# Kernel optimization log

Hardware: AMD Instinct MI355X
Metric: run time of the kernel (lower is better)

The kernel has to match this reference:

```python
import jax, jax.numpy as jnp
import numpy as np

EPS = 1e-6
SLOPE = 0.01  # torch LeakyReLU / VNLeakyReLU default negative_slope
B = 1024      # number of graphs (segments)
N, S, V, H = 120000, 256, 64, 64


def _vn(W, x):
    # VNLinear: channel-mixing linear on (N, C, 3) vector features, W: (O, C)
    return jnp.einsum('oc,ncd->nod', W, x)


def _gv_linear(Wv1, Wv2, Ws, Wg, bg, sca, vec):
    # GVLinear: vec -> hidden vec, concat |vec| with sca, gate out_vec by sigmoid(out_sca)
    vi = _vn(Wv1, vec)                                   # (N, Hid, 3)
    vnorm = jnp.linalg.norm(vi, axis=-1)                 # (N, Hid)
    out_sca = jnp.concatenate([vnorm, sca], axis=-1) @ Ws.T   # (N, out_sca)
    out_vec = _vn(Wv2, vi)                               # (N, out_vec, 3)
    gate = jax.nn.sigmoid(out_sca @ Wg.T + bg)[..., None]
    return out_sca, gate * out_vec


def _vn_lrelu(Wd, x):
    # VNLeakyReLU: direction-gated leaky relu on vector channels
    d = _vn(Wd, x)
    dot = jnp.sum(x * d, axis=-1, keepdims=True)
    dsq = jnp.sum(d * d, axis=-1, keepdims=True)
    mask = (dot >= 0).astype(x.dtype)
    proj = x - (dot / (dsq + EPS)) * d
    return SLOPE * x + (1.0 - SLOPE) * (mask * x + (1.0 - mask) * proj)


def _lrelu(x):
    return jnp.where(x >= 0, x, SLOPE * x)


def setup_inputs() -> dict:
    key = jax.random.key(0)
    ks = jax.random.split(key, 40)
    g = lambda i, shape, s=1.0: jax.random.normal(ks[i], shape, dtype=jnp.float32) * s
    w = 0.06  # ~1/sqrt(fan_in) for fan_in 256-320
    inp = {
        'h_sca': g(0, (N, S)),
        'h_vec': g(1, (N, V, 3)),
        'pos_context': g(2, (N, 3), 3.0),
        'time_embed': g(3, (100, S), 0.05),
        # att_net: GVPerceptronVN(256,64 -> 256,64)
        'att1_Wv1': g(4, (H, V), 0.12), 'att1_Wv2': g(5, (H, H), 0.12),
        'att1_Ws': g(6, (S, S + H), w), 'att1_Wg': g(7, (H, S), w), 'att1_bg': g(8, (H,), 0.01),
        'att1_Wd': g(9, (H, H), 0.12),
        # att_net: GVLinear(256,64 -> 1,1), dim_hid = max(64,1) = 64
        'att2_Wv1': g(10, (H, H), 0.12), 'att2_Wv2': g(11, (1, H), 0.12),
        'att2_Ws': g(12, (1, S + H), w), 'att2_Wg': g(13, (1, 1), 0.5), 'att2_bg': g(14, (1,), 0.01),
        # net: GVPerceptronVN(256,64 -> 256,64)
        'net1_Wv1': g(15, (H, V), 0.12), 'net1_Wv2': g(16, (H, H), 0.12),
        'net1_Ws': g(17, (S, S + H), w), 'net1_Wg': g(18, (H, S), w), 'net1_bg': g(19, (H,), 0.01),
        'net1_Wd': g(20, (H, H), 0.12),
        # net: GVLinear(256,64 -> 256,64)
        'net2_Wv1': g(21, (H, H), 0.12), 'net2_Wv2': g(22, (S - (S - V), H), 0.12).reshape(V, H),
        'net2_Ws': g(23, (S, S + H), w), 'net2_Wg': g(24, (V, S), w), 'net2_bg': g(25, (V,), 0.01),
        't': 17,
        'batch_id': jnp.sort(jax.random.randint(ks[30], (N,), 0, B)),
    }
    return inp


def reference(h_sca, h_vec, pos_context, time_embed,
              att1_Wv1, att1_Wv2, att1_Ws, att1_Wg, att1_bg, att1_Wd,
              att2_Wv1, att2_Wv2, att2_Ws, att2_Wg, att2_bg,
              net1_Wv1, net1_Wv2, net1_Ws, net1_Wg, net1_bg, net1_Wd,
              net2_Wv1, net2_Wv2, net2_Ws, net2_Wg, net2_bg,
              t, batch_id):
    sca = h_sca + time_embed[t]          # same timestep embedding broadcast to all N nodes
    vec = h_vec

    # attention branch: GVPerceptronVN -> GVLinear(...,1,1), keep scalar output
    s, v = _gv_linear(att1_Wv1, att1_Wv2, att1_Ws, att1_Wg, att1_bg, sca, vec)
    s, v = _lrelu(s), _vn_lrelu(att1_Wd, v)
    att, _ = _gv_linear(att2_Wv1, att2_Wv2, att2_Ws, att2_Wg, att2_bg, s, v)  # (N,1)

    # feature branch: GVPerceptronVN -> GVLinear(...,in_sca,in_vec)
    s2, v2 = _gv_linear(net1_Wv1, net1_Wv2, net1_Ws, net1_Wg, net1_bg, sca, vec)
    s2, v2 = _lrelu(s2), _vn_lrelu(net1_Wd, v2)
    fs, fv = _gv_linear(net2_Wv1, net2_Wv2, net2_Ws, net2_Wg, net2_bg, s2, v2)

    # scatter_softmax over batch_id segments
    m = jax.ops.segment_max(att, batch_id, num_segments=B)
    e = jnp.exp(att - m[batch_id])
    z = jax.ops.segment_sum(e, batch_id, num_segments=B)
    w = e / z[batch_id]                  # (N,1)

    pos_focal = jax.ops.segment_sum(w * pos_context, batch_id, num_segments=B)   # (B,3)
    feat_focal = jax.ops.segment_sum(w * fs, batch_id, num_segments=B)           # (B,256)
    vec_focal = jax.ops.segment_sum(w[:, :, None] * fv, batch_id, num_segments=B)  # (B,64,3)
    return feat_focal, vec_focal, pos_focal
```

## Files before the change

kernel.cpp:

```cpp
#include <hip/hip_runtime.h>
#include <hip/hip_bf16.h>
#include <math.h>

#define NN 120000
#define NT 32
#define TPB 512
#define NBLK (NN / NT)
#define BSEG 1024

typedef __attribute__((ext_vector_type(8))) short short8;
typedef __attribute__((ext_vector_type(16))) float floatx16;

#define OFF_A1_WV1 0
#define OFF_A1_WV2 4096
#define OFF_A1_WS  8192
#define OFF_A1_WG  90112
#define OFF_A1_WD  106496
#define OFF_A2_WV1 110592
#define OFF_N1_WV1 114688
#define OFF_N1_WV2 118784
#define OFF_N1_WS  122880
#define OFF_N1_WG  204800
#define OFF_N1_WD  221184
#define OFF_N2_WV1 225280
#define OFF_N2_WV2 229376
#define OFF_N2_WS  233472
#define OFF_N2_WG  315392
#define W_TOTAL    331776

__device__ __forceinline__ unsigned short f2bf(float x) {
  __hip_bfloat16 b = __float2bfloat16(x);
  return __builtin_bit_cast(unsigned short, b);
}
__device__ __forceinline__ unsigned int f2bf2(float lo, float hi) {
  return (unsigned int)f2bf(lo) | ((unsigned int)f2bf(hi) << 16);
}
__device__ __forceinline__ float bf2f(unsigned short h) {
  return __uint_as_float(((unsigned int)h) << 16);
}
__device__ __forceinline__ float bflo(unsigned int u) { return __uint_as_float(u << 16); }
__device__ __forceinline__ float bfhi(unsigned int u) { return __uint_as_float(u & 0xffff0000u); }

struct P {
  const float *h_sca, *h_vec, *pos, *te;
  const float *a1_bg, *n1_bg, *n2_bg, *a2_Ws;
  const int *t, *bid;
  const unsigned short* wb;
  float *att, *w, *out;
};


struct CvtP { const float* src[15]; unsigned short* dst; };

__global__ __launch_bounds__(256) void cvt_kernel(CvtP c) {
  const int sizes[15] = {4096, 4096, 81920, 16384, 4096, 4096,
                         4096, 4096, 81920, 16384, 4096,
                         4096, 4096, 81920, 16384};
  int idx = blockIdx.x * 256 + threadIdx.x;
  if (idx >= W_TOTAL) return;
  int seg = 0, off = 0;
  while (idx - off >= sizes[seg]) { off += sizes[seg]; ++seg; }
  c.dst[idx] = f2bf(c.src[seg][idx - off]);
}


__device__ __forceinline__ void stage(const P& p, unsigned short* sS, unsigned short* sV,
                                      const float* te_row, int node0, int tid) {
  int i = tid >> 4, j = tid & 15;
  {
    int c0 = j * 16;
    const float4* src = (const float4*)&p.h_sca[(node0 + i) * 256 + c0];
    const float4* te4 = (const float4*)&te_row[c0];
    float4 a0 = src[0], b0 = te4[0];
    float4 a1 = src[1], b1 = te4[1];
    float4 a2 = src[2], b2 = te4[2];
    float4 a3 = src[3], b3 = te4[3];
    uint4 o0 = make_uint4(f2bf2(a0.x + b0.x, a0.y + b0.y), f2bf2(a0.z + b0.z, a0.w + b0.w),
                          f2bf2(a1.x + b1.x, a1.y + b1.y), f2bf2(a1.z + b1.z, a1.w + b1.w));
    uint4 o1 = make_uint4(f2bf2(a2.x + b2.x, a2.y + b2.y), f2bf2(a2.z + b2.z, a2.w + b2.w),
                          f2bf2(a3.x + b3.x, a3.y + b3.y), f2bf2(a3.z + b3.z, a3.w + b3.w));
    *(uint4*)&sS[i * 264 + c0] = o0;
    *(uint4*)&sS[i * 264 + c0 + 8] = o1;
  }
  {
    int c0 = j * 4;
    const float4* src = (const float4*)&p.h_vec[(node0 + i) * 192 + c0 * 3];
    float4 v0 = src[0], v1 = src[1], v2 = src[2];
    int b = (i * 3) * 72 + c0;
    *(uint2*)&sV[b]       = make_uint2(f2bf2(v0.x, v0.w), f2bf2(v1.z, v2.y));
    *(uint2*)&sV[b + 72]  = make_uint2(f2bf2(v0.y, v1.x), f2bf2(v1.w, v2.z));
    *(uint2*)&sV[b + 144] = make_uint2(f2bf2(v0.z, v1.y), f2bf2(v2.x, v2.w));
  }
}

__device__ __forceinline__ void big_gemm(const unsigned short* __restrict__ Wb,
                                         const unsigned short* sVN,
                                         const unsigned short* sX,
                                         unsigned short* sDst,
                                         int wid, int lane) {
  const int m = lane & 31, h = lane >> 5;
  const int n0 = wid * 32;
  const unsigned short* wrow = Wb + (n0 + m) * 320 + h * 8;
  short8 B[20];
#pragma unroll
  for (int k = 0; k < 8; ++k) B[k] = *(const short8*)&wrow[k * 16];
  floatx16 acc0 = {}, acc1 = {};
#pragma unroll
  for (int k = 0; k < 20; k += 2) {
    if (k + 8 < 20) B[k + 8] = *(const short8*)&wrow[(k + 8) * 16];
    if (k + 9 < 20) B[k + 9] = *(const short8*)&wrow[(k + 9) * 16];
    short8 a0, a1;
    if (k < 4)     a0 = *(const short8*)&sVN[m * 72 + k * 16 + h * 8];
    else           a0 = *(const short8*)&sX[m * 264 + (k - 4) * 16 + h * 8];
    if (k + 1 < 4) a1 = *(const short8*)&sVN[m * 72 + (k + 1) * 16 + h * 8];
    else           a1 = *(const short8*)&sX[m * 264 + (k - 3) * 16 + h * 8];
    acc0 = __builtin_amdgcn_mfma_f32_32x32x16_bf16(a0, B[k], acc0, 0, 0, 0);
    acc1 = __builtin_amdgcn_mfma_f32_32x32x16_bf16(a1, B[k + 1], acc1, 0, 0, 0);
  }
  __syncthreads();
#pragma unroll
  for (int r = 0; r < 16; ++r) {
    int row = (r & 3) + 8 * (r >> 2) + 4 * h;
    sDst[row * 264 + n0 + m] = f2bf(acc0[r] + acc1[r]);
  }
}

__device__ __forceinline__ void gate_gemm(const unsigned short* __restrict__ Wg,
                                          const float* __restrict__ bg,
                                          const unsigned short* sX,
                                          unsigned short* sG, int wid, int lane) {
  const int m = lane & 31, h = lane >> 5;
  const int n0 = wid * 32;
  const unsigned short* wrow = Wg + (n0 + m) * 256 + h * 8;
  short8 B[16];
#pragma unroll
  for (int k = 0; k < 8; ++k) B[k] = *(const short8*)&wrow[k * 16];
  float bb = bg[n0 + m];
  floatx16 acc0 = {}, acc1 = {};
#pragma unroll
  for (int k = 0; k < 16; k += 2) {
    if (k + 8 < 16) B[k + 8] = *(const short8*)&wrow[(k + 8) * 16];
    if (k + 9 < 16) B[k + 9] = *(const short8*)&wrow[(k + 9) * 16];
    short8 a0 = *(const short8*)&sX[m * 264 + k * 16 + h * 8];
    short8 a1 = *(const short8*)&sX[m * 264 + k * 16 + 16 + h * 8];
    acc0 = __builtin_amdgcn_mfma_f32_32x32x16_bf16(a0, B[k], acc0, 0, 0, 0);
    acc1 = __builtin_amdgcn_mfma_f32_32x32x16_bf16(a1, B[k + 1], acc1, 0, 0, 0);
  }
#pragma unroll
  for (int r = 0; r < 16; ++r) {
    int i = (r & 3) + 8 * (r >> 2) + 4 * h;
    float v = acc0[r] + acc1[r] + bb;
    sG[i * 64 + n0 + m] = f2bf(__builtin_amdgcn_rcpf(1.f + __expf(-v)));
  }
}

__device__ __forceinline__ void vecmm(const unsigned short* __restrict__ Wb,
                                      const unsigned short* sSrc,
                                      unsigned short* sDst,
                                      int wid, int lane) {
  if (wid >= 6) return;
  const int m = lane & 31, h = lane >> 5;
  const int nd0 = (wid >> 1) * 32, o0 = (wid & 1) * 32;
  const unsigned short* wrow = Wb + (o0 + m) * 64 + h * 8;
  short8 b0 = *(const short8*)&wrow[0];
  short8 b1 = *(const short8*)&wrow[16];
  short8 b2 = *(const short8*)&wrow[32];
  short8 b3 = *(const short8*)&wrow[48];
  floatx16 acc = {};
#pragma unroll
  for (int k0 = 0; k0 < 64; k0 += 16) {
    short8 a = *(const short8*)&sSrc[(nd0 + m) * 72 + k0 + h * 8];
    short8 b = (k0 == 0) ? b0 : (k0 == 16) ? b1 : (k0 == 32) ? b2 : b3;
    acc = __builtin_amdgcn_mfma_f32_32x32x16_bf16(a, b, acc, 0, 0, 0);
  }
#pragma unroll
  for (int r = 0; r < 16; ++r) {
    int nd = nd0 + (r & 3) + 8 * (r >> 2) + 4 * h;
    sDst[nd * 72 + o0 + m] = f2bf(acc[r]);
  }
}

__device__ __forceinline__ void vnorm(const unsigned short* sV, unsigned short* sVN, int tid) {
  if (tid >= 256) return;
  int i = tid >> 3, c0 = (tid & 7) * 8;
  int b = (i * 3) * 72 + c0;
  short8 vx = *(const short8*)&sV[b];
  short8 vy = *(const short8*)&sV[b + 72];
  short8 vz = *(const short8*)&sV[b + 144];
  unsigned int o[4];
#pragma unroll
  for (int q = 0; q < 4; ++q) {
    float x0 = bf2f((unsigned short)vx[2 * q]),     y0 = bf2f((unsigned short)vy[2 * q]),     z0 = bf2f((unsigned short)vz[2 * q]);
    float x1 = bf2f((unsigned short)vx[2 * q + 1]), y1 = bf2f((unsigned short)vy[2 * q + 1]), z1 = bf2f((unsigned short)vz[2 * q + 1]);
    o[q] = f2bf2(sqrtf(x0 * x0 + y0 * y0 + z0 * z0), sqrtf(x1 * x1 + y1 * y1 + z1 * z1));
  }
  *(uint4*)&sVN[i * 72 + c0] = make_uint4(o[0], o[1], o[2], o[3]);
}

__device__ __forceinline__ void gatemul(unsigned short* sVx, const unsigned short* sG, int tid) {
  if (tid >= 256) return;
  int i = tid >> 3, c0 = (tid & 7) * 8;
  short8 g = *(const short8*)&sG[i * 64 + c0];
  float gf[8];
#pragma unroll
  for (int j = 0; j < 8; ++j) gf[j] = bf2f((unsigned short)g[j]);
  int b = (i * 3) * 72 + c0;
#pragma unroll
  for (int d = 0; d < 3; ++d) {
    short8 v = *(const short8*)&sVx[b + d * 72];
    unsigned int o[4];
#pragma unroll
    for (int q = 0; q < 4; ++q)
      o[q] = f2bf2(bf2f((unsigned short)v[2 * q]) * gf[2 * q],
                   bf2f((unsigned short)v[2 * q + 1]) * gf[2 * q + 1]);
    *(uint4*)&sVx[b + d * 72] = make_uint4(o[0], o[1], o[2], o[3]);
  }
}

__device__ __forceinline__ void vn_lrelu(unsigned short* sVx, const unsigned short* sVd, int tid) {
  if (tid >= 256) return;
  int i = tid >> 3, c0 = (tid & 7) * 8;
  int b = (i * 3) * 72 + c0;
  short8 x0 = *(const short8*)&sVx[b];
  short8 x1 = *(const short8*)&sVx[b + 72];
  short8 x2 = *(const short8*)&sVx[b + 144];
  short8 d0 = *(const short8*)&sVd[b];
  short8 d1 = *(const short8*)&sVd[b + 72];
  short8 d2 = *(const short8*)&sVd[b + 144];
  float rx[8], ry[8], rz[8];
#pragma unroll
  for (int j = 0; j < 8; ++j) {
    float a0 = bf2f((unsigned short)x0[j]), a1 = bf2f((unsigned short)x1[j]), a2 = bf2f((unsigned short)x2[j]);
    float e0 = bf2f((unsigned short)d0[j]), e1 = bf2f((unsigned short)d1[j]), e2 = bf2f((unsigned short)d2[j]);
    float dot = a0 * e0 + a1 * e1 + a2 * e2;
    float dsq = e0 * e0 + e1 * e1 + e2 * e2;
    float f = dot >= 0.f ? 0.f : 0.99f * dot * __builtin_amdgcn_rcpf(dsq + 1e-6f);
    rx[j] = a0 - f * e0; ry[j] = a1 - f * e1; rz[j] = a2 - f * e2;
  }
  unsigned int ox[4], oy[4], oz[4];
#pragma unroll
  for (int q = 0; q < 4; ++q) {
    ox[q] = f2bf2(rx[2 * q], rx[2 * q + 1]);
    oy[q] = f2bf2(ry[2 * q], ry[2 * q + 1]);
    oz[q] = f2bf2(rz[2 * q], rz[2 * q + 1]);
  }
  *(uint4*)&sVx[b]       = make_uint4(ox[0], ox[1], ox[2], ox[3]);
  *(uint4*)&sVx[b + 72]  = make_uint4(oy[0], oy[1], oy[2], oy[3]);
  *(uint4*)&sVx[b + 144] = make_uint4(oz[0], oz[1], oz[2], oz[3]);
}

__device__ __forceinline__ void lrelu_vec(unsigned short* sS, int u, int nthr) {
  for (int cc = u; cc < NT * 32; cc += nthr) {
    int i = cc >> 5, off = (cc & 31) * 8;
    short8 v = *(short8*)&sS[i * 264 + off];
    unsigned int o[4];
#pragma unroll
    for (int q = 0; q < 4; ++q) {
      float a = bf2f((unsigned short)v[2 * q]);
      float b = bf2f((unsigned short)v[2 * q + 1]);
      a = a >= 0.f ? a : 0.01f * a;
      b = b >= 0.f ? b : 0.01f * b;
      o[q] = f2bf2(a, b);
    }
    *(uint4*)&sS[i * 264 + off] = make_uint4(o[0], o[1], o[2], o[3]);
  }
}

__device__ __forceinline__ float* out_addr(float* out, int b, int f) {
  if (f < 256) return out + b * 256 + f;
  if (f < 448) return out + 1024 * 256 + b * 192 + (f - 256);
  return out + 1024 * 256 + 1024 * 192 + b * 3 + (f - 448);
}


__global__ __launch_bounds__(TPB, 6) void att_kernel(P p) {
  __shared__ unsigned short sS[NT * 264];
  __shared__ unsigned short sVA[96 * 72], sVB[96 * 72];
  __shared__ unsigned short sGN[2304];
  unsigned short* sVN = sGN;
  unsigned short* sG = sGN;
  int tid = threadIdx.x, wid = tid >> 6, lane = tid & 63;
  int node0 = blockIdx.x * NT;
  const unsigned short* wb = p.wb;

  stage(p, sS, sVA, p.te + p.t[0] * 256, node0, tid); __syncthreads();
  vecmm(wb + OFF_A1_WV1, sVA, sVB, wid, lane); __syncthreads();
  vnorm(sVB, sVN, tid); __syncthreads();
  big_gemm(wb + OFF_A1_WS, sVN, sS, sS, wid, lane); __syncthreads();
  if (wid < 2) gate_gemm(wb + OFF_A1_WG, p.a1_bg, sS, sG, wid, lane);
  else vecmm(wb + OFF_A1_WV2, sVB, sVA, wid - 2, lane);
  __syncthreads();
  gatemul(sVA, sG, tid); __syncthreads();
  vecmm(wb + OFF_A1_WD, sVA, sVB, wid, lane); __syncthreads();
  vn_lrelu(sVA, sVB, tid); __syncthreads();
  vecmm(wb + OFF_A2_WV1, sVA, sVB, wid, lane); __syncthreads();

  int i = tid >> 4, j = tid & 15;
  float part = 0.f;
  {
    int c0 = j * 4;
    uint2 wx = *(const uint2*)&sVB[(i * 3 + 0) * 72 + c0];
    uint2 wy = *(const uint2*)&sVB[(i * 3 + 1) * 72 + c0];
    uint2 wz = *(const uint2*)&sVB[(i * 3 + 2) * 72 + c0];
    float4 ws = *(const float4*)&p.a2_Ws[c0];
    float n0 = sqrtf(bflo(wx.x) * bflo(wx.x) + bflo(wy.x) * bflo(wy.x) + bflo(wz.x) * bflo(wz.x));
    float n1 = sqrtf(bfhi(wx.x) * bfhi(wx.x) + bfhi(wy.x) * bfhi(wy.x) + bfhi(wz.x) * bfhi(wz.x));
    float n2 = sqrtf(bflo(wx.y) * bflo(wx.y) + bflo(wy.y) * bflo(wy.y) + bflo(wz.y) * bflo(wz.y));
    float n3 = sqrtf(bfhi(wx.y) * bfhi(wx.y) + bfhi(wy.y) * bfhi(wy.y) + bfhi(wz.y) * bfhi(wz.y));
    part = fmaf(ws.x, n0, part);
    part = fmaf(ws.y, n1, part);
    part = fmaf(ws.z, n2, part);
    part = fmaf(ws.w, n3, part);
  }
  {
    int k0 = j * 16;
    short8 s0 = *(const short8*)&sS[i * 264 + k0];
    short8 s1 = *(const short8*)&sS[i * 264 + k0 + 8];
    const float4* wp = (const float4*)&p.a2_Ws[64 + k0];
#pragma unroll
    for (int q = 0; q < 4; ++q) {
      float4 w4 = wp[q];
      float vv[4];
#pragma unroll
      for (int e = 0; e < 4; ++e) {
        short raw = (q < 2) ? ((q == 0) ? s0[e] : s0[4 + e]) : ((q == 2) ? s1[e] : s1[4 + e]);
        float x = bf2f((unsigned short)raw);
        vv[e] = x >= 0.f ? x : 0.01f * x;
      }
      part = fmaf(w4.x, vv[0], part);
      part = fmaf(w4.y, vv[1], part);
      part = fmaf(w4.z, vv[2], part);
      part = fmaf(w4.w, vv[3], part);
    }
  }
  part += __shfl_down(part, 8, 16);
  part += __shfl_down(part, 4, 16);
  part += __shfl_down(part, 2, 16);
  part += __shfl_down(part, 1, 16);
  if (j == 0) p.att[node0 + i] = part;
}


__global__ __launch_bounds__(256) void softmax_kernel(const float* __restrict__ att,
                                                      const int* __restrict__ bid,
                                                      float* __restrict__ w) {
  __shared__ float red[256];
  __shared__ float s_m, s_z;
  int b = blockIdx.x, tid = threadIdx.x;
  int lo = 0, hi = NN;
  while (lo < hi) { int mid = (lo + hi) >> 1; if (bid[mid] < b) lo = mid + 1; else hi = mid; }
  int start = lo;
  hi = NN;
  while (lo < hi) { int mid = (lo + hi) >> 1; if (bid[mid] < b + 1) lo = mid + 1; else hi = mid; }
  int end = lo;

  float m = -1e30f;
  for (int i = start + tid; i < end; i += 256) m = fmaxf(m, att[i]);
  red[tid] = m; __syncthreads();
  for (int s = 128; s > 0; s >>= 1) { if (tid < s) red[tid] = fmaxf(red[tid], red[tid + s]); __syncthreads(); }
  if (tid == 0) s_m = red[0];
  __syncthreads();
  m = s_m;
  float z = 0.f;
  for (int i = start + tid; i < end; i += 256) z += __expf(att[i] - m);
  red[tid] = z; __syncthreads();
  for (int s = 128; s > 0; s >>= 1) { if (tid < s) red[tid] += red[tid + s]; __syncthreads(); }
  if (tid == 0) s_z = red[0];
  __syncthreads();
  float inv = 1.f / s_z;
  for (int i = start + tid; i < end; i += 256) w[i] = __expf(att[i] - m) * inv;
}


__global__ __launch_bounds__(TPB, 6) void net_kernel(P p) {
  __shared__ unsigned short sS[NT * 264];
  __shared__ unsigned short sVA[96 * 72], sVB[96 * 72];
  __shared__ unsigned short sGN[2304];
  __shared__ float s_w[NT];
  __shared__ float s_pos[NT * 3];
  __shared__ int s_bid[NT];
  unsigned short* sVN = sGN;
  unsigned short* sG = sGN;
  int tid = threadIdx.x, wid = tid >> 6, lane = tid & 63;
  int node0 = blockIdx.x * NT;
  const unsigned short* wb = p.wb;

  stage(p, sS, sVA, p.te + p.t[0] * 256, node0, tid); __syncthreads();
  vecmm(wb + OFF_N1_WV1, sVA, sVB, wid, lane);
  if (wid >= 6) {
    int u = tid - 384;
    if (u < NT) { s_w[u] = p.w[node0 + u]; s_bid[u] = p.bid[node0 + u]; }
    for (int v = u; v < NT * 3; v += 128) s_pos[v] = p.pos[node0 * 3 + v];
  }
  __syncthreads();
  vnorm(sVB, sVN, tid); __syncthreads();
  big_gemm(wb + OFF_N1_WS, sVN, sS, sS, wid, lane); __syncthreads();
  if (wid < 2) gate_gemm(wb + OFF_N1_WG, p.n1_bg, sS, sG, wid, lane);
  else vecmm(wb + OFF_N1_WV2, sVB, sVA, wid - 2, lane);
  __syncthreads();
  if (tid < 256) gatemul(sVA, sG, tid);
  else lrelu_vec(sS, tid - 256, 256);
  __syncthreads();
  vecmm(wb + OFF_N1_WD, sVA, sVB, wid, lane); __syncthreads();
  vn_lrelu(sVA, sVB, tid); __syncthreads();
  vecmm(wb + OFF_N2_WV1, sVA, sVB, wid, lane); __syncthreads();
  vnorm(sVB, sVN, tid); __syncthreads();
  big_gemm(wb + OFF_N2_WS, sVN, sS, sS, wid, lane); __syncthreads();
  if (wid < 2) gate_gemm(wb + OFF_N2_WG, p.n2_bg, sS, sG, wid, lane);
  else vecmm(wb + OFF_N2_WV2, sVB, sVA, wid - 2, lane);
  __syncthreads();

  if (tid < 451) {
    int f = tid;
    float acc = 0.f;
    int cur = s_bid[0];
    int c = 0, d = 0;
    if (f >= 256 && f < 448) { int r = f - 256; c = r / 3; d = r - c * 3; }
    for (int i2 = 0; i2 < NT; ++i2) {
      int sg = s_bid[i2];
      if (sg != cur) { atomicAdd(out_addr(p.out, cur, f), acc); acc = 0.f; cur = sg; }
      float val;
      if (f < 256) val = bf2f(sS[i2 * 264 + f]);
      else if (f < 448)
        val = bf2f(sVA[(i2 * 3 + d) * 72 + c]) * bf2f(sG[i2 * 64 + c]);
      else val = s_pos[i2 * 3 + (f - 448)];
      acc = fmaf(s_w[i2], val, acc);
    }
    atomicAdd(out_addr(p.out, cur, f), acc);
  }
}


extern "C" void kernel_launch(void* const* d_in, const int* in_sizes, int n_in,
                              void* d_out, int out_size, void* d_ws, size_t ws_size,
                              hipStream_t stream) {
  float* ws = (float*)d_ws;
  unsigned short* wb = (unsigned short*)(ws + 2 * NN);

  CvtP c;
  c.src[0]  = (const float*)d_in[4];
  c.src[1]  = (const float*)d_in[5];
  c.src[2]  = (const float*)d_in[6];
  c.src[3]  = (const float*)d_in[7];
  c.src[4]  = (const float*)d_in[9];
  c.src[5]  = (const float*)d_in[10];
  c.src[6]  = (const float*)d_in[15];
  c.src[7]  = (const float*)d_in[16];
  c.src[8]  = (const float*)d_in[17];
  c.src[9]  = (const float*)d_in[18];
  c.src[10] = (const float*)d_in[20];
  c.src[11] = (const float*)d_in[21];
  c.src[12] = (const float*)d_in[22];
  c.src[13] = (const float*)d_in[23];
  c.src[14] = (const float*)d_in[24];
  c.dst = wb;

  P p;
  p.h_sca = (const float*)d_in[0];
  p.h_vec = (const float*)d_in[1];
  p.pos   = (const float*)d_in[2];
  p.te    = (const float*)d_in[3];
  p.a1_bg = (const float*)d_in[8];
  p.a2_Ws = (const float*)d_in[12];
  p.n1_bg = (const float*)d_in[19];
  p.n2_bg = (const float*)d_in[25];
  p.t   = (const int*)d_in[26];
  p.bid = (const int*)d_in[27];
  p.wb  = wb;
  p.att = ws;
  p.w   = ws + NN;
  p.out = (float*)d_out;

  hipMemsetAsync(d_out, 0, (size_t)out_size * sizeof(float), stream);
  cvt_kernel<<<(W_TOTAL + 255) / 256, 256, 0, stream>>>(c);
  att_kernel<<<NBLK, TPB, 0, stream>>>(p);
  softmax_kernel<<<BSEG, 256, 0, stream>>>(p.att, p.bid, p.w);
  net_kernel<<<NBLK, TPB, 0, stream>>>(p);
}
```

Measured before the change: 670.3 us.

## Double node tile to 64 with 1024-thread blocks and dynamic LDS

Raises the per-block node tile from 32 to 64 and threads per block from 512 to 1024. The GEMM helpers take extra row-block offsets so each weight fragment loaded from global memory serves twice as many nodes, and LDS becomes a single dynamic buffer with explicit offsets. The segment-sum epilogue splits each feature across two threads, one per half of the tile. The cost is more LDS per block and fewer resident blocks per CU, and the tile is hard-coded around the stage/att paths, some of which are not shown and may not all have been updated for 64 nodes.

```diff
diff --git a/kernel.cpp b/kernel.cpp
--- a/kernel.cpp
+++ b/kernel.cpp
@@ -3,10 +3,17 @@
 #include <math.h>
 
 #define NN 120000
-#define NT 32
-#define TPB 512
+#define NT 64
+#define TPB 1024
 #define NBLK (NN / NT)
 #define BSEG 1024
+
+#define L_SS   0
+#define L_SVA  16896
+#define L_SVB  30720
+#define L_SGN  44544
+#define L_END  49152
+#define LDS_BYTES (98304 + 64*4 + 192*4 + 64*4)
 
 typedef __attribute__((ext_vector_type(8))) short short8;
 typedef __attribute__((ext_vector_type(16))) float floatx16;
@@ -99,7 +106,8 @@
                                          unsigned short* sDst,
                                          int wid, int lane) {
   const int m = lane & 31, h = lane >> 5;
-  const int n0 = wid * 32;
+  const int n0 = (wid & 7) * 32, mb = (wid >> 3) * 32;
+  const int ar = mb + m;
   const unsigned short* wrow = Wb + (n0 + m) * 320 + h * 8;
   short8 B[20];
 #pragma unroll
@@ -110,17 +118,17 @@
     if (k + 8 < 20) B[k + 8] = *(const short8*)&wrow[(k + 8) * 16];
     if (k + 9 < 20) B[k + 9] = *(const short8*)&wrow[(k + 9) * 16];
     short8 a0, a1;
-    if (k < 4)     a0 = *(const short8*)&sVN[m * 72 + k * 16 + h * 8];
-    else           a0 = *(const short8*)&sX[m * 264 + (k - 4) * 16 + h * 8];
-    if (k + 1 < 4) a1 = *(const short8*)&sVN[m * 72 + (k + 1) * 16 + h * 8];
-    else           a1 = *(const short8*)&sX[m * 264 + (k - 3) * 16 + h * 8];
+    if (k < 4)     a0 = *(const short8*)&sVN[ar * 72 + k * 16 + h * 8];
+    else           a0 = *(const short8*)&sX[ar * 264 + (k - 4) * 16 + h * 8];
+    if (k + 1 < 4) a1 = *(const short8*)&sVN[ar * 72 + (k + 1) * 16 + h * 8];
+    else           a1 = *(const short8*)&sX[ar * 264 + (k - 3) * 16 + h * 8];
     acc0 = __builtin_amdgcn_mfma_f32_32x32x16_bf16(a0, B[k], acc0, 0, 0, 0);
     acc1 = __builtin_amdgcn_mfma_f32_32x32x16_bf16(a1, B[k + 1], acc1, 0, 0, 0);
   }
   __syncthreads();
 #pragma unroll
   for (int r = 0; r < 16; ++r) {
-    int row = (r & 3) + 8 * (r >> 2) + 4 * h;
+    int row = mb + (r & 3) + 8 * (r >> 2) + 4 * h;
     sDst[row * 264 + n0 + m] = f2bf(acc0[r] + acc1[r]);
   }
 }
@@ -128,9 +136,9 @@
 __device__ __forceinline__ void gate_gemm(const unsigned short* __restrict__ Wg,
                                           const float* __restrict__ bg,
                                           const unsigned short* sX,
-                                          unsigned short* sG, int wid, int lane) {
+                                          unsigned short* sG, int job, int lane) {
   const int m = lane & 31, h = lane >> 5;
-  const int n0 = wid * 32;
+  const int n0 = (job & 1) * 32, mb = (job >> 1) * 32;
   const unsigned short* wrow = Wg + (n0 + m) * 256 + h * 8;
   short8 B[16];
 #pragma unroll
@@ -141,14 +149,14 @@
   for (int k = 0; k < 16; k += 2) {
     if (k + 8 < 16) B[k + 8] = *(const short8*)&wrow[(k + 8) * 16];
     if (k + 9 < 16) B[k + 9] = *(const short8*)&wrow[(k + 9) * 16];
-    short8 a0 = *(const short8*)&sX[m * 264 + k * 16 + h * 8];
-    short8 a1 = *(const short8*)&sX[m * 264 + k * 16 + 16 + h * 8];
+    short8 a0 = *(const short8*)&sX[(mb + m) * 264 + k * 16 + h * 8];
+    short8 a1 = *(const short8*)&sX[(mb + m) * 264 + k * 16 + 16 + h * 8];
     acc0 = __builtin_amdgcn_mfma_f32_32x32x16_bf16(a0, B[k], acc0, 0, 0, 0);
     acc1 = __builtin_amdgcn_mfma_f32_32x32x16_bf16(a1, B[k + 1], acc1, 0, 0, 0);
   }
 #pragma unroll
   for (int r = 0; r < 16; ++r) {
-    int i = (r & 3) + 8 * (r >> 2) + 4 * h;
+    int i = mb + (r & 3) + 8 * (r >> 2) + 4 * h;
     float v = acc0[r] + acc1[r] + bb;
     sG[i * 64 + n0 + m] = f2bf(__builtin_amdgcn_rcpf(1.f + __expf(-v)));
   }
@@ -157,10 +165,10 @@
 __device__ __forceinline__ void vecmm(const unsigned short* __restrict__ Wb,
                                       const unsigned short* sSrc,
                                       unsigned short* sDst,
-                                      int wid, int lane) {
-  if (wid >= 6) return;
+                                      int job, int lane) {
+  if (job >= 12) return;
   const int m = lane & 31, h = lane >> 5;
-  const int nd0 = (wid >> 1) * 32, o0 = (wid & 1) * 32;
+  const int nd0 = (job >> 1) * 32, o0 = (job & 1) * 32;
   const unsigned short* wrow = Wb + (o0 + m) * 64 + h * 8;
   short8 b0 = *(const short8*)&wrow[0];
   short8 b1 = *(const short8*)&wrow[16];
@@ -181,7 +189,7 @@
 }
 
 __device__ __forceinline__ void vnorm(const unsigned short* sV, unsigned short* sVN, int tid) {
-  if (tid >= 256) return;
+  if (tid >= NT * 8) return;
   int i = tid >> 3, c0 = (tid & 7) * 8;
   int b = (i * 3) * 72 + c0;
   short8 vx = *(const short8*)&sV[b];
@@ -198,7 +206,7 @@
 }
 
 __device__ __forceinline__ void gatemul(unsigned short* sVx, const unsigned short* sG, int tid) {
-  if (tid >= 256) return;
+  if (tid >= NT * 8) return;
   int i = tid >> 3, c0 = (tid & 7) * 8;
   short8 g = *(const short8*)&sG[i * 64 + c0];
   float gf[8];
@@ -218,7 +226,7 @@
 }
 
 __device__ __forceinline__ void vn_lrelu(unsigned short* sVx, const unsigned short* sVd, int tid) {
-  if (tid >= 256) return;
+  if (tid >= NT * 8) return;
   int i = tid >> 3, c0 = (tid & 7) * 8;
   int b = (i * 3) * 72 + c0;
   short8 x0 = *(const short8*)&sVx[b];
@@ -273,10 +281,12 @@
 }
 
 
-__global__ __launch_bounds__(TPB, 6) void att_kernel(P p) {
-  __shared__ unsigned short sS[NT * 264];
-  __shared__ unsigned short sVA[96 * 72], sVB[96 * 72];
-  __shared__ unsigned short sGN[2304];
+__global__ __launch_bounds__(TPB, 4) void att_kernel(P p) {
+  extern __shared__ unsigned short smem[];
+  unsigned short* sS  = smem + L_SS;
+  unsigned short* sVA = smem + L_SVA;
+  unsigned short* sVB = smem + L_SVB;
+  unsigned short* sGN = smem + L_SGN;
   unsigned short* sVN = sGN;
   unsigned short* sG = sGN;
   int tid = threadIdx.x, wid = tid >> 6, lane = tid & 63;
@@ -287,8 +297,8 @@
   vecmm(wb + OFF_A1_WV1, sVA, sVB, wid, lane); __syncthreads();
   vnorm(sVB, sVN, tid); __syncthreads();
   big_gemm(wb + OFF_A1_WS, sVN, sS, sS, wid, lane); __syncthreads();
-  if (wid < 2) gate_gemm(wb + OFF_A1_WG, p.a1_bg, sS, sG, wid, lane);
-  else vecmm(wb + OFF_A1_WV2, sVB, sVA, wid - 2, lane);
+  if (wid < 4) gate_gemm(wb + OFF_A1_WG, p.a1_bg, sS, sG, wid, lane);
+  else vecmm(wb + OFF_A1_WV2, sVB, sVA, wid - 4, lane);
   __syncthreads();
   gatemul(sVA, sG, tid); __syncthreads();
   vecmm(wb + OFF_A1_WD, sVA, sVB, wid, lane); __syncthreads();
@@ -372,61 +382,63 @@
 }
 
 
-__global__ __launch_bounds__(TPB, 6) void net_kernel(P p) {
-  __shared__ unsigned short sS[NT * 264];
-  __shared__ unsigned short sVA[96 * 72], sVB[96 * 72];
-  __shared__ unsigned short sGN[2304];
-  __shared__ float s_w[NT];
-  __shared__ float s_pos[NT * 3];
-  __shared__ int s_bid[NT];
+__global__ __launch_bounds__(TPB, 4) void net_kernel(P p) {
+  extern __shared__ unsigned short smem[];
+  unsigned short* sS  = smem + L_SS;
+  unsigned short* sVA = smem + L_SVA;
+  unsigned short* sVB = smem + L_SVB;
+  unsigned short* sGN = smem + L_SGN;
+  float* s_w   = (float*)(smem + L_END);
+  float* s_pos = s_w + NT;
+  int*   s_bid = (int*)(s_pos + NT * 3);
   unsigned short* sVN = sGN;
   unsigned short* sG = sGN;
   int tid = threadIdx.x, wid = tid >> 6, lane = tid & 63;
   int node0 = blockIdx.x * NT;
   const unsigned short* wb = p.wb;
 
-  stage(p, sS, sVA, p.te + p.t[0] * 256, node0, tid); __syncthreads();
-  vecmm(wb + OFF_N1_WV1, sVA, sVB, wid, lane);
-  if (wid >= 6) {
-    int u = tid - 384;
-    if (u < NT) { s_w[u] = p.w[node0 + u]; s_bid[u] = p.bid[node0 + u]; }
-    for (int v = u; v < NT * 3; v += 128) s_pos[v] = p.pos[node0 * 3 + v];
-  }
-  __syncthreads();
+  stage(p, sS, sVA, p.te + p.t[0] * 256, node0, tid);
+  if (tid < NT) { s_w[tid] = p.w[node0 + tid]; s_bid[tid] = p.bid[node0 + tid]; }
+  else if (tid >= 256 && tid < 256 + NT * 3) s_pos[tid - 256] = p.pos[node0 * 3 + (tid - 256)];
+  __syncthreads();
+  vecmm(wb + OFF_N1_WV1, sVA, sVB, wid, lane); __syncthreads();
   vnorm(sVB, sVN, tid); __syncthreads();
   big_gemm(wb + OFF_N1_WS, sVN, sS, sS, wid, lane); __syncthreads();
-  if (wid < 2) gate_gemm(wb + OFF_N1_WG, p.n1_bg, sS, sG, wid, lane);
-  else vecmm(wb + OFF_N1_WV2, sVB, sVA, wid - 2, lane);
-  __syncthreads();
-  if (tid < 256) gatemul(sVA, sG, tid);
-  else lrelu_vec(sS, tid - 256, 256);
+  if (wid < 4) gate_gemm(wb + OFF_N1_WG, p.n1_bg, sS, sG, wid, lane);
+  else vecmm(wb + OFF_N1_WV2, sVB, sVA, wid - 4, lane);
+  __syncthreads();
+  if (tid < NT * 8) gatemul(sVA, sG, tid);
+  else lrelu_vec(sS, tid - NT * 8, TPB - NT * 8);
   __syncthreads();
   vecmm(wb + OFF_N1_WD, sVA, sVB, wid, lane); __syncthreads();
   vn_lrelu(sVA, sVB, tid); __syncthreads();
   vecmm(wb + OFF_N2_WV1, sVA, sVB, wid, lane); __syncthreads();
   vnorm(sVB, sVN, tid); __syncthreads();
   big_gemm(wb + OFF_N2_WS, sVN, sS, sS, wid, lane); __syncthreads();
-  if (wid < 2) gate_gemm(wb + OFF_N2_WG, p.n2_bg, sS, sG, wid, lane);
-  else vecmm(wb + OFF_N2_WV2, sVB, sVA, wid - 2, lane);
-  __syncthreads();
-
-  if (tid < 451) {
-    int f = tid;
-    float acc = 0.f;
-    int cur = s_bid[0];
-    int c = 0, d = 0;
-    if (f >= 256 && f < 448) { int r = f - 256; c = r / 3; d = r - c * 3; }
-    for (int i2 = 0; i2 < NT; ++i2) {
-      int sg = s_bid[i2];
-      if (sg != cur) { atomicAdd(out_addr(p.out, cur, f), acc); acc = 0.f; cur = sg; }
-      float val;
-      if (f < 256) val = bf2f(sS[i2 * 264 + f]);
-      else if (f < 448)
-        val = bf2f(sVA[(i2 * 3 + d) * 72 + c]) * bf2f(sG[i2 * 64 + c]);
-      else val = s_pos[i2 * 3 + (f - 448)];
-      acc = fmaf(s_w[i2], val, acc);
+  if (wid < 4) gate_gemm(wb + OFF_N2_WG, p.n2_bg, sS, sG, wid, lane);
+  else vecmm(wb + OFF_N2_WV2, sVB, sVA, wid - 4, lane);
+  __syncthreads();
+
+  {
+    int f = tid >> 1, half = tid & 1;
+    if (f < 451) {
+      int i0 = half * 32, i1 = i0 + 32;
+      float acc = 0.f;
+      int cur = s_bid[i0];
+      int c = 0, d = 0;
+      if (f >= 256 && f < 448) { int r = f - 256; c = r / 3; d = r - c * 3; }
+      for (int i2 = i0; i2 < i1; ++i2) {
+        int sg = s_bid[i2];
+        if (sg != cur) { atomicAdd(out_addr(p.out, cur, f), acc); acc = 0.f; cur = sg; }
+        float val;
+        if (f < 256) val = bf2f(sS[i2 * 264 + f]);
+        else if (f < 448)
+          val = bf2f(sVA[(i2 * 3 + d) * 72 + c]) * bf2f(sG[i2 * 64 + c]);
+        else val = s_pos[i2 * 3 + (f - 448)];
+        acc = fmaf(s_w[i2], val, acc);
+      }
+      atomicAdd(out_addr(p.out, cur, f), acc);
     }
-    atomicAdd(out_addr(p.out, cur, f), acc);
   }
 }
 
@@ -436,6 +448,15 @@
                               hipStream_t stream) {
   float* ws = (float*)d_ws;
   unsigned short* wb = (unsigned short*)(ws + 2 * NN);
+
+  static bool attr_done = false;
+  if (!attr_done) {
+    hipFuncSetAttribute((const void*)att_kernel,
+                        hipFuncAttributeMaxDynamicSharedMemorySize, LDS_BYTES);
+    hipFuncSetAttribute((const void*)net_kernel,
+                        hipFuncAttributeMaxDynamicSharedMemorySize, LDS_BYTES);
+    attr_done = true;
+  }
 
   CvtP c;
   c.src[0]  = (const float*)d_in[4];
@@ -473,7 +494,7 @@
 
   hipMemsetAsync(d_out, 0, (size_t)out_size * sizeof(float), stream);
   cvt_kernel<<<(W_TOTAL + 255) / 256, 256, 0, stream>>>(c);
-  att_kernel<<<NBLK, TPB, 0, stream>>>(p);
+  att_kernel<<<NBLK, TPB, LDS_BYTES, stream>>>(p);
   softmax_kernel<<<BSEG, 256, 0, stream>>>(p.att, p.bid, p.w);
-  net_kernel<<<NBLK, TPB, 0, stream>>>(p);
-}
+  net_kernel<<<NBLK, TPB, LDS_BYTES, stream>>>(p);
+}
```

Result: slower. 833.7 us (+24.4%).
